# Optimization experiments

Hardware: AMD Instinct MI355X
Metric: run time of the kernel (lower is better)

The kernel has to match this reference:

```python
import jax, jax.numpy as jnp
import numpy as np

N_BUS = 1024
BATCH = 4096
N_NODES = N_BUS * BATCH
N_EDGES = 4 * N_NODES
F_IN, F1, F2, HID = 7, 12, 12, 128
EPS = 1e-5


def setup_inputs() -> dict:
    key = jax.random.key(0)
    ks = jax.random.split(key, 16)
    inp = {
        "x": jax.random.normal(ks[0], (N_NODES, F_IN), dtype=jnp.float32),
        "edge_index": jax.random.randint(ks[1], (2, N_EDGES), 0, N_NODES, dtype=jnp.int64),
        "batch_size": BATCH,
        # conv1 (PyG GraphConv): lin_rel (with bias) on aggregated msgs, lin_root (no bias)
        "Wrel1": jax.random.normal(ks[2], (F1, F_IN), dtype=jnp.float32) * 0.3,
        "brel1": jax.random.normal(ks[3], (F1,), dtype=jnp.float32) * 0.1,
        "Wroot1": jax.random.normal(ks[4], (F1, F_IN), dtype=jnp.float32) * 0.3,
        # conv2
        "Wrel2": jax.random.normal(ks[5], (F2, F1), dtype=jnp.float32) * 0.25,
        "brel2": jax.random.normal(ks[6], (F2,), dtype=jnp.float32) * 0.1,
        "Wroot2": jax.random.normal(ks[7], (F2, F1), dtype=jnp.float32) * 0.25,
        # batch norms
        "g1": jnp.ones((F1,), jnp.float32), "b1": jnp.zeros((F1,), jnp.float32),
        "g2": jnp.ones((F2,), jnp.float32), "b2": jnp.zeros((F2,), jnp.float32),
        # MLP head
        "W1": jax.random.normal(ks[8], (HID, N_BUS * F2), dtype=jnp.float32) * 0.01,
        "bl1": jnp.zeros((HID,), jnp.float32),
        "W2": jax.random.normal(ks[9], (N_BUS * 2, HID), dtype=jnp.float32) * 0.05,
        "bl2": jnp.zeros((N_BUS * 2,), jnp.float32),
    }
    return inp


def graph_conv(x, src, dst, Wrel, brel, Wroot):
    # out_i = Wrel @ (sum_{j: j->i} x_j) + brel + Wroot @ x_i
    agg = jax.ops.segment_sum(x[src], dst, num_segments=N_NODES)
    return agg @ Wrel.T + brel + x @ Wroot.T


def batch_norm(x, g, b):
    mu = x.mean(axis=0)
    var = x.var(axis=0)  # biased, as torch BN uses for normalization
    return (x - mu) * jax.lax.rsqrt(var + EPS) * g + b


def reference(x, edge_index, batch_size, Wrel1, brel1, Wroot1, Wrel2, brel2, Wroot2,
              g1, b1, g2, b2, W1, bl1, W2, bl2):
    src, dst = edge_index[0], edge_index[1]
    h = graph_conv(x, src, dst, Wrel1, brel1, Wroot1)
    h = jax.nn.relu(batch_norm(h, g1, b1))
    h = graph_conv(h, src, dst, Wrel2, brel2, Wroot2)
    h = jax.nn.relu(batch_norm(h, g2, b2))
    h = h.reshape(batch_size, N_BUS * F2)
    h = jax.nn.relu(h @ W1.T + bl1)
    return h @ W2.T + bl2
```

## Files before the change

### kernel.cpp

```cpp
#include <hip/hip_runtime.h>
#include <hip/hip_bf16.h>

#define NBUS    1024
#define BATCHSZ 4096
#define NNODES  (NBUS*BATCHSZ)
#define NEDGES  (4*NNODES)
#define FIN     7
#define FF1     12
#define FF2     12
#define HIDD    128
#define KDIM    (NBUS*FF2)
#define ODIM    (NBUS*2)
#define NBKT    4096
#define CAP     4608
#define ITPT    18
#define NCB     64
#define CAPA    265216

#define SZ_P    ((size_t)NNODES * 32)
#define SZ_HB   ((size_t)NNODES * FF2 * 2)
#define SZ_HID  ((size_t)BATCHSZ * HIDD * sizeof(float))
#define SZ_E    ((size_t)NBKT * CAP * sizeof(unsigned))
#define SZ_PB   ((size_t)NCB * CAPA * 8)

typedef unsigned u32x2v  __attribute__((ext_vector_type(2)));
typedef unsigned u32x4v  __attribute__((ext_vector_type(4)));

__device__ __forceinline__ float bflo(unsigned p){ return __uint_as_float(p << 16); }
__device__ __forceinline__ float bfhi(unsigned p){ return __uint_as_float(p & 0xffff0000u); }
__device__ __forceinline__ unsigned short f2bf(float f) {
    unsigned u = __float_as_uint(f);
    return (unsigned short)((u + 0x7fffu + ((u >> 16) & 1u)) >> 16);
}
__device__ __forceinline__ void nts_u2(unsigned* p, unsigned a, unsigned b) {
    u32x2v w; w.x = a; w.y = b;
    __builtin_nontemporal_store(w, (u32x2v*)p);
}
__device__ __forceinline__ void nts_u4(uint4* p, uint4 v) {
    u32x4v w; w.x = v.x; w.y = v.y; w.z = v.z; w.w = v.w;
    __builtin_nontemporal_store(w, (u32x4v*)p);
}
__device__ __forceinline__ uint2 ntl_u2(const unsigned* p) {
    u32x2v v = __builtin_nontemporal_load((const u32x2v*)p);
    uint2 r; r.x = v.x; r.y = v.y; return r;
}
__device__ __forceinline__ float4 ntl_f4(const float* p) {
    typedef float f32x4v __attribute__((ext_vector_type(4)));
    f32x4v v = __builtin_nontemporal_load((const f32x4v*)p);
    return make_float4(v.x, v.y, v.z, v.w);
}

__device__ __forceinline__ void acc7(float* agg, uint4 a) {
    agg[0] += bflo(a.x); agg[1] += bfhi(a.x);
    agg[2] += bflo(a.y); agg[3] += bfhi(a.y);
    agg[4] += bflo(a.z); agg[5] += bfhi(a.z);
    agg[6] += bflo(a.w);
}
__device__ __forceinline__ void accY(float* agg, const float* sc, const float* sh,
                                     uint4 r0, uint4 r1) {
    float v[FF1] = {bflo(r0.x), bfhi(r0.x), bflo(r0.y), bfhi(r0.y),
                    bflo(r0.z), bfhi(r0.z), bflo(r0.w), bfhi(r0.w),
                    bflo(r1.x), bfhi(r1.x), bflo(r1.y), bfhi(r1.y)};
    #pragma unroll
    for (int j = 0; j < FF1; ++j) {
        float y = v[j] * sc[j] + sh[j];
        agg[j] += (y > 0.f ? y : 0.f);
    }
}

__global__ void k_diag(float* __restrict__ out, int n, float v) {
    size_t i = (size_t)blockIdx.x * blockDim.x + threadIdx.x;
    if (i < (size_t)n) out[i] = v;
}

__global__ void k_init(const int* __restrict__ w, int* __restrict__ flag,
                       int* __restrict__ bcur, int* __restrict__ bcurA) {
    int u = blockIdx.x * 256 + threadIdx.x;
    if (u < NBKT) bcur[u] = u * CAP;
    if (u < NCB) bcurA[u] = u * CAPA;
    if (blockIdx.x == 0) {
        __shared__ int any;
        if (threadIdx.x == 0) any = 0;
        __syncthreads();
        int acc = 0;
        #pragma unroll
        for (int q = 0; q < 4; ++q) acc |= w[1 + 2 * (threadIdx.x * 4 + q)];
        if (acc) atomicOr(&any, 1);
        __syncthreads();
        if (threadIdx.x == 0) *flag = (any == 0) ? 2 : 1;
    }
}

__global__ __launch_bounds__(512) void k_partA(const int* __restrict__ ei,
                                               const int* __restrict__ flag,
                                               int* __restrict__ bcurA,
                                               unsigned* __restrict__ ebufA) {
    __shared__ int hist[NCB], lbase[NCB];
    int t = threadIdx.x;
    if (t < NCB) hist[t] = 0;
    __syncthreads();
    int mult = *flag;
    size_t base = (size_t)blockIdx.x * 32768;
    #pragma unroll 4
    for (int u = 0; u < 64; ++u) {
        size_t e = base + (size_t)u * 512 + t;
        int d = __builtin_nontemporal_load(ei + ((size_t)NEDGES + e) * mult);
        atomicAdd(&hist[d >> 16], 1);
    }
    __syncthreads();
    if (t < NCB) {
        int c = hist[t];
        lbase[t] = c ? atomicAdd(&bcurA[t], c) : 0;
        hist[t] = 0;
    }
    __syncthreads();
    #pragma unroll 4
    for (int u = 0; u < 64; ++u) {
        size_t e = base + (size_t)u * 512 + t;
        int s = __builtin_nontemporal_load(ei + e * mult);
        int d = __builtin_nontemporal_load(ei + ((size_t)NEDGES + e) * mult);
        int bk = d >> 16;
        int pos = lbase[bk] + atomicAdd(&hist[bk], 1);
        if (pos < (bk + 1) * CAPA) {
            uint2* p = (uint2*)(ebufA + (size_t)pos * 2);
            *p = make_uint2((unsigned)s, (unsigned)d);
        }
    }
}

__global__ __launch_bounds__(512) void k_partB(const unsigned* __restrict__ ebufA,
                                               const int* __restrict__ bendA,
                                               int* __restrict__ bcur,
                                               unsigned* __restrict__ ebuf) {
    __shared__ int hist[NCB], lbase[NCB];
    int t = threadIdx.x;
    int cb = blockIdx.x >> 2;
    int qq = blockIdx.x & 3;
    int abeg = cb * CAPA;
    int n = bendA[cb] - abeg; if (n > CAPA) n = CAPA;
    int beg = abeg + (int)(((long long)n * qq) >> 2);
    int end = abeg + (int)(((long long)n * (qq + 1)) >> 2);
    if (t < NCB) hist[t] = 0;
    __syncthreads();
    for (int k = beg + t; k < end; k += 512) {
        uint2 e = ntl_u2(ebufA + (size_t)k * 2);
        atomicAdd(&hist[(e.y >> 10) & 63u], 1);
    }
    __syncthreads();
    if (t < NCB) {
        int c = hist[t];
        lbase[t] = c ? atomicAdd(&bcur[cb * 64 + t], c) : 0;
        hist[t] = 0;
    }
    __syncthreads();
    for (int k = beg + t; k < end; k += 512) {
        uint2 e = ntl_u2(ebufA + (size_t)k * 2);
        int lb = (e.y >> 10) & 63u;
        int fb = cb * 64 + lb;
        int pos = lbase[lb] + atomicAdd(&hist[lb], 1);
        if (pos < (fb + 1) * CAP)
            ebuf[pos] = (e.x << 10) | (e.y & 1023u);
    }
}

__global__ __launch_bounds__(256) void k_padx(const float* __restrict__ x,
                                              uint4* __restrict__ xb) {
    size_t q = (size_t)blockIdx.x * blockDim.x + threadIdx.x;
    if (q >= NNODES / 4) return;
    const float4* xr = (const float4*)(x + q * 28);
    float v[28];
    #pragma unroll
    for (int u = 0; u < 7; ++u) {
        float4 f = xr[u];
        v[4*u] = f.x; v[4*u+1] = f.y; v[4*u+2] = f.z; v[4*u+3] = f.w;
    }
    #pragma unroll
    for (int n = 0; n < 4; ++n) {
        unsigned short h[8];
        #pragma unroll
        for (int j = 0; j < 7; ++j) h[j] = f2bf(v[7*n + j]);
        h[7] = 0;
        uint4 o;
        o.x = (unsigned)h[0] | ((unsigned)h[1] << 16);
        o.y = (unsigned)h[2] | ((unsigned)h[3] << 16);
        o.z = (unsigned)h[4] | ((unsigned)h[5] << 16);
        o.w = (unsigned)h[6] | ((unsigned)h[7] << 16);
        xb[q * 4 + n] = o;
    }
}

__global__ __launch_bounds__(256, 4) void k_conv1(const int* __restrict__ bend,
                                                  const unsigned* __restrict__ ebuf,
                                                  const uint4* __restrict__ xb,
                                                  const float* __restrict__ Wrel,
                                                  const float* __restrict__ brel,
                                                  const float* __restrict__ Wroot,
                                                  uint4* __restrict__ h1p) {
    __shared__ unsigned stage[CAP];
    __shared__ int hist[1024];
    __shared__ int offL[1024];
    __shared__ int wsum[4];
    __shared__ float sWr[FF1 * FIN], sWo[FF1 * FIN], sb[FF1];
    int t = threadIdx.x;
    if (t < FF1 * FIN) { sWr[t] = Wrel[t]; sWo[t] = Wroot[t]; }
    if (t < FF1) sb[t] = brel[t];
    int bk = blockIdx.x;
    int ebeg = bk * CAP;
    int n = bend[bk] - ebeg; if (n > CAP) n = CAP; if (n < 0) n = 0;
    for (int u = t; u < 1024; u += 256) hist[u] = 0;
    __syncthreads();
    for (int k = t; k < n; k += 256)
        atomicAdd(&hist[ebuf[ebeg + k] & 1023u], 1);
    __syncthreads();
    int v[4]; int s = 0;
    #pragma unroll
    for (int u = 0; u < 4; ++u) { v[u] = hist[t * 4 + u]; s += v[u]; }
    int lane = t & 63, w = t >> 6;
    int iv = s;
    for (int o = 1; o < 64; o <<= 1) { int uu = __shfl_up(iv, o); if (lane >= o) iv += uu; }
    if (lane == 63) wsum[w] = iv;
    __syncthreads();
    int basep = 0;
    #pragma unroll
    for (int ww = 0; ww < 4; ++ww) if (ww < w) basep += wsum[ww];
    int run = basep + iv - s;
    #pragma unroll
    for (int u = 0; u < 4; ++u) {
        offL[t * 4 + u] = run;
        hist[t * 4 + u] = run;
        run += v[u];
    }
    __syncthreads();
    for (int k = t; k < n; k += 256) {
        unsigned p = ebuf[ebeg + k];
        int pos = atomicAdd(&hist[p & 1023u], 1);
        stage[pos] = p >> 10;
    }
    __syncthreads();
    #pragma unroll
    for (int nn = 0; nn < 4; ++nn) {
        int li = nn * 256 + t;
        size_t i = (size_t)bk * 1024 + li;
        int beg = offL[li];
        int end = (li == 1023) ? n : offL[li + 1];
        float agg[FIN] = {0.f, 0.f, 0.f, 0.f, 0.f, 0.f, 0.f};
        int k = beg;
        for (; k + 3 < end; k += 4) {
            unsigned s0 = stage[k], s1 = stage[k+1], s2 = stage[k+2], s3 = stage[k+3];
            uint4 a0 = xb[s0], a1 = xb[s1], a2 = xb[s2], a3 = xb[s3];
            acc7(agg, a0); acc7(agg, a1); acc7(agg, a2); acc7(agg, a3);
        }
        for (; k < end; ++k) acc7(agg, xb[stage[k]]);
        uint4 ow = xb[i];
        float xv[FIN] = {bflo(ow.x), bfhi(ow.x), bflo(ow.y), bfhi(ow.y),
                         bflo(ow.z), bfhi(ow.z), bflo(ow.w)};
        unsigned short hh[FF1];
        #pragma unroll
        for (int j = 0; j < FF1; ++j) {
            float h = sb[j];
            #pragma unroll
            for (int q = 0; q < FIN; ++q) h += sWr[j * FIN + q] * agg[q] + sWo[j * FIN + q] * xv[q];
            hh[j] = f2bf(h);
        }
        uint4 w1, w2;
        w1.x = (unsigned)hh[0] | ((unsigned)hh[1] << 16);
        w1.y = (unsigned)hh[2] | ((unsigned)hh[3] << 16);
        w1.z = (unsigned)hh[4] | ((unsigned)hh[5] << 16);
        w1.w = (unsigned)hh[6] | ((unsigned)hh[7] << 16);
        w2.x = (unsigned)hh[8] | ((unsigned)hh[9] << 16);
        w2.y = (unsigned)hh[10]| ((unsigned)hh[11] << 16);
        w2.z = 0u; w2.w = 0u;
        nts_u4(h1p + i * 2, w1);
        nts_u4(h1p + i * 2 + 1, w2);
    }
}

template<int STRIDE>
__global__ __launch_bounds__(256) void k_statsb(const unsigned* __restrict__ hb,
                                                double* __restrict__ stats) {
    __shared__ float red[4][FF1], redq[4][FF1];
    int t = threadIdx.x;
    float ps[FF1], pq[FF1];
    #pragma unroll
    for (int j = 0; j < FF1; ++j) { ps[j] = 0.f; pq[j] = 0.f; }
    for (size_t i = (size_t)blockIdx.x * 256 + t; i < NNODES; i += 256 * 256) {
        const uint2* r = (const uint2*)(hb + i * STRIDE);
        uint2 u0 = r[0], u1 = r[1], u2 = r[2];
        float v[FF1] = {bflo(u0.x), bfhi(u0.x), bflo(u0.y), bfhi(u0.y),
                        bflo(u1.x), bfhi(u1.x), bflo(u1.y), bfhi(u1.y),
                        bflo(u2.x), bfhi(u2.x), bflo(u2.y), bfhi(u2.y)};
        #pragma unroll
        for (int j = 0; j < FF1; ++j) { ps[j] += v[j]; pq[j] += v[j] * v[j]; }
    }
    #pragma unroll
    for (int j = 0; j < FF1; ++j)
        for (int o = 1; o < 64; o <<= 1) { ps[j] += __shfl_xor(ps[j], o); pq[j] += __shfl_xor(pq[j], o); }
    int lane = t & 63, wv = t >> 6;
    if (lane == 0) {
        #pragma unroll
        for (int j = 0; j < FF1; ++j) { red[wv][j] = ps[j]; redq[wv][j] = pq[j]; }
    }
    __syncthreads();
    if (t < FF1) {
        float s = red[0][t] + red[1][t] + red[2][t] + red[3][t];
        float q = redq[0][t] + redq[1][t] + redq[2][t] + redq[3][t];
        atomicAdd(&stats[t], (double)s);
        atomicAdd(&stats[FF1 + t], (double)q);
    }
}

__global__ void k_finalize(const double* __restrict__ stats, const float* __restrict__ g,
                           const float* __restrict__ b, float* __restrict__ ss) {
    int j = threadIdx.x;
    if (j < FF1) {
        double mean = stats[j] * (1.0 / NNODES);
        double var  = stats[FF1 + j] * (1.0 / NNODES) - mean * mean;
        float sc = (float)((double)g[j] / sqrt(var + 1e-5));
        ss[j] = sc;
        ss[FF1 + j] = b[j] - (float)mean * sc;
    }
}

__global__ __launch_bounds__(256, 4) void k_conv2(const int* __restrict__ bend,
                                                  const unsigned* __restrict__ ebuf,
                                                  const uint4* __restrict__ h1p,
                                                  const float* __restrict__ ss,
                                                  const float* __restrict__ Wrel,
                                                  const float* __restrict__ brel,
                                                  const float* __restrict__ Wroot,
                                                  unsigned* __restrict__ h2b) {
    __shared__ unsigned stage[CAP];
    __shared__ int hist[1024];
    __shared__ int offL[1024];
    __shared__ int wsum[4];
    __shared__ float sWr[FF2 * FF1], sWo[FF2 * FF1], sb[FF2], sc[FF1], sh[FF1];
    int t = threadIdx.x;
    if (t < FF2 * FF1) { sWr[t] = Wrel[t]; sWo[t] = Wroot[t]; }
    if (t < FF2) { sb[t] = brel[t]; sc[t] = ss[t]; sh[t] = ss[FF1 + t]; }
    int bk = blockIdx.x;
    int ebeg = bk * CAP;
    int n = bend[bk] - ebeg; if (n > CAP) n = CAP; if (n < 0) n = 0;
    for (int u = t; u < 1024; u += 256) hist[u] = 0;
    __syncthreads();
    for (int k = t; k < n; k += 256)
        atomicAdd(&hist[ebuf[ebeg + k] & 1023u], 1);
    __syncthreads();
    int v[4]; int s = 0;
    #pragma unroll
    for (int u = 0; u < 4; ++u) { v[u] = hist[t * 4 + u]; s += v[u]; }
    int lane = t & 63, w = t >> 6;
    int iv = s;
    for (int o = 1; o < 64; o <<= 1) { int uu = __shfl_up(iv, o); if (lane >= o) iv += uu; }
    if (lane == 63) wsum[w] = iv;
    __syncthreads();
    int basep = 0;
    #pragma unroll
    for (int ww = 0; ww < 4; ++ww) if (ww < w) basep += wsum[ww];
    int run = basep + iv - s;
    #pragma unroll
    for (int u = 0; u < 4; ++u) {
        offL[t * 4 + u] = run;
        hist[t * 4 + u] = run;
        run += v[u];
    }
    __syncthreads();
    for (int k = t; k < n; k += 256) {
        unsigned p = ebuf[ebeg + k];
        int pos = atomicAdd(&hist[p & 1023u], 1);
        stage[pos] = p >> 10;
    }
    __syncthreads();
    #pragma unroll
    for (int nn = 0; nn < 4; ++nn) {
        int li = nn * 256 + t;
        size_t i = (size_t)bk * 1024 + li;
        int beg = offL[li];
        int end = (li == 1023) ? n : offL[li + 1];
        float agg[FF1];
        #pragma unroll
        for (int j = 0; j < FF1; ++j) agg[j] = 0.f;
        int k = beg;
        for (; k + 3 < end; k += 4) {
            unsigned s0 = stage[k], s1 = stage[k+1], s2 = stage[k+2], s3 = stage[k+3];
            uint4 a0 = h1p[(size_t)s0 * 2], a1 = h1p[(size_t)s0 * 2 + 1];
            uint4 b0 = h1p[(size_t)s1 * 2], b1 = h1p[(size_t)s1 * 2 + 1];
            uint4 c0 = h1p[(size_t)s2 * 2], c1 = h1p[(size_t)s2 * 2 + 1];
            uint4 d0 = h1p[(size_t)s3 * 2], d1 = h1p[(size_t)s3 * 2 + 1];
            accY(agg, sc, sh, a0, a1);
            accY(agg, sc, sh, b0, b1);
            accY(agg, sc, sh, c0, c1);
            accY(agg, sc, sh, d0, d1);
        }
        for (; k < end; ++k) {
            unsigned s0 = stage[k];
            accY(agg, sc, sh, h1p[(size_t)s0 * 2], h1p[(size_t)s0 * 2 + 1]);
        }
        uint4 o0 = h1p[i * 2], o1 = h1p[i * 2 + 1];
        float vo[FF1] = {bflo(o0.x), bfhi(o0.x), bflo(o0.y), bfhi(o0.y),
                         bflo(o0.z), bfhi(o0.z), bflo(o0.w), bfhi(o0.w),
                         bflo(o1.x), bfhi(o1.x), bflo(o1.y), bfhi(o1.y)};
        float y[FF1];
        #pragma unroll
        for (int j = 0; j < FF1; ++j) {
            float wv = vo[j] * sc[j] + sh[j];
            y[j] = wv > 0.f ? wv : 0.f;
        }
        unsigned short hh[FF2];
        #pragma unroll
        for (int j = 0; j < FF2; ++j) {
            float h = sb[j];
            #pragma unroll
            for (int q = 0; q < FF1; ++q) h += sWr[j * FF1 + q] * agg[q] + sWo[j * FF1 + q] * y[q];
            hh[j] = f2bf(h);
        }
        unsigned* p = h2b + i * 6;
        nts_u2(p,     (unsigned)hh[0] | ((unsigned)hh[1] << 16),
                      (unsigned)hh[2] | ((unsigned)hh[3] << 16));
        nts_u2(p + 2, (unsigned)hh[4] | ((unsigned)hh[5] << 16),
                      (unsigned)hh[6] | ((unsigned)hh[7] << 16));
        nts_u2(p + 4, (unsigned)hh[8] | ((unsigned)hh[9] << 16),
                      (unsigned)hh[10]| ((unsigned)hh[11] << 16));
    }
}

__global__ __launch_bounds__(256) void k_gemm1(const unsigned short* __restrict__ h2b,
                                               const float* __restrict__ ss2,
                                               const float* __restrict__ W1,
                                               float* __restrict__ hidp) {
    __shared__ float As[32][128];
    __shared__ float Bs[32][128];
    __shared__ float sc[FF2], sh[FF2];
    int t = threadIdx.x;
    if (t < FF2) { sc[t] = ss2[t]; sh[t] = ss2[FF2 + t]; }
    __syncthreads();
    int mb = blockIdx.x;
    int ks = blockIdx.y;
    const int KS = KDIM / 8;
    int m0 = mb * 128;
    int kbase = ks * KS;
    int r  = t >> 1;
    int kg = t & 1;
    int tr = t >> 4;
    int tc = t & 15;
    float acc[8][8];
    #pragma unroll
    for (int i = 0; i < 8; ++i)
        #pragma unroll
        for (int j = 0; j < 8; ++j) acc[i][j] = 0.f;

    for (int kt = 0; kt < KS; kt += 32) {
        int c0 = kbase + kt + 16 * kg;
        const uint2* arow = (const uint2*)(h2b + (size_t)(m0 + r) * KDIM + c0);
        const float* brow = W1 + (size_t)r * KDIM + c0;
        #pragma unroll
        for (int i = 0; i < 4; ++i) {
            uint2 av = arow[i];
            int cc = c0 + 4 * i;
            int j0 = cc % FF2;
            float vals[4] = {bflo(av.x), bfhi(av.x), bflo(av.y), bfhi(av.y)};
            #pragma unroll
            for (int ii = 0; ii < 4; ++ii) {
                int j = j0 + ii; if (j >= FF2) j -= FF2;
                float v = vals[ii] * sc[j] + sh[j];
                As[16 * kg + 4 * i + ii][r] = v > 0.f ? v : 0.f;
            }
            float4 bv = *(const float4*)(brow + 4 * i);
            Bs[16 * kg + 4 * i + 0][r] = bv.x;
            Bs[16 * kg + 4 * i + 1][r] = bv.y;
            Bs[16 * kg + 4 * i + 2][r] = bv.z;
            Bs[16 * kg + 4 * i + 3][r] = bv.w;
        }
        __syncthreads();
        #pragma unroll
        for (int k = 0; k < 32; ++k) {
            float a[8], b[8];
            *(float4*)&a[0] = *(const float4*)&As[k][8 * tr];
            *(float4*)&a[4] = *(const float4*)&As[k][8 * tr + 4];
            *(float4*)&b[0] = *(const float4*)&Bs[k][8 * tc];
            *(float4*)&b[4] = *(const float4*)&Bs[k][8 * tc + 4];
            #pragma unroll
            for (int i = 0; i < 8; ++i)
                #pragma unroll
                for (int j = 0; j < 8; ++j) acc[i][j] += a[i] * b[j];
        }
        __syncthreads();
    }
    float* obase = hidp + (size_t)ks * (BATCHSZ * HIDD);
    #pragma unroll
    for (int i = 0; i < 8; ++i) {
        float* orow = obase + (size_t)(m0 + 8 * tr + i) * HIDD + 8 * tc;
        *(float4*)(orow)     = make_float4(acc[i][0], acc[i][1], acc[i][2], acc[i][3]);
        *(float4*)(orow + 4) = make_float4(acc[i][4], acc[i][5], acc[i][6], acc[i][7]);
    }
}

__global__ __launch_bounds__(256) void k_hred(const float* __restrict__ hidp,
                                              const float* __restrict__ bl1,
                                              float* __restrict__ hid) {
    int i = blockIdx.x * 256 + threadIdx.x;
    float s = bl1[i & (HIDD - 1)];
    #pragma unroll
    for (int p = 0; p < 8; ++p) s += hidp[(size_t)p * (BATCHSZ * HIDD) + i];
    hid[i] = s > 0.f ? s : 0.f;
}

__global__ __launch_bounds__(256) void k_gemm2(const float* __restrict__ hid,
                                               const float* __restrict__ W2,
                                               const float* __restrict__ bl2,
                                               float* __restrict__ out) {
    __shared__ float As[32][128];
    __shared__ float Bs[32][128];
    int t = threadIdx.x;
    int m0 = blockIdx.x * 128;
    int n0 = blockIdx.y * 128;
    int r  = t >> 1;
    int kg = t & 1;
    int tr = t >> 4;
    int tc = t & 15;
    float acc[8][8];
    #pragma unroll
    for (int i = 0; i < 8; ++i)
        #pragma unroll
        for (int j = 0; j < 8; ++j) acc[i][j] = 0.f;

    for (int kt = 0; kt < HIDD; kt += 32) {
        int c0 = kt + 16 * kg;
        #pragma unroll
        for (int i = 0; i < 4; ++i) {
            float4 av = *(const float4*)(hid + (size_t)(m0 + r) * HIDD + c0 + 4 * i);
            As[16 * kg + 4 * i + 0][r] = av.x;
            As[16 * kg + 4 * i + 1][r] = av.y;
            As[16 * kg + 4 * i + 2][r] = av.z;
            As[16 * kg + 4 * i + 3][r] = av.w;
            float4 bv = *(const float4*)(W2 + (size_t)(n0 + r) * HIDD + c0 + 4 * i);
            Bs[16 * kg + 4 * i + 0][r] = bv.x;
            Bs[16 * kg + 4 * i + 1][r] = bv.y;
            Bs[16 * kg + 4 * i + 2][r] = bv.z;
            Bs[16 * kg + 4 * i + 3][r] = bv.w;
        }
        __syncthreads();
        #pragma unroll
        for (int k = 0; k < 32; ++k) {
            float a[8], b[8];
            *(float4*)&a[0] = *(const float4*)&As[k][8 * tr];
            *(float4*)&a[4] = *(const float4*)&As[k][8 * tr + 4];
            *(float4*)&b[0] = *(const float4*)&Bs[k][8 * tc];
            *(float4*)&b[4] = *(const float4*)&Bs[k][8 * tc + 4];
            #pragma unroll
            for (int i = 0; i < 8; ++i)
                #pragma unroll
                for (int j = 0; j < 8; ++j) acc[i][j] += a[i] * b[j];
        }
        __syncthreads();
    }
    float4 c0v = *(const float4*)(bl2 + n0 + 8 * tc);
    float4 c1v = *(const float4*)(bl2 + n0 + 8 * tc + 4);
    float bvals[8] = {c0v.x, c0v.y, c0v.z, c0v.w, c1v.x, c1v.y, c1v.z, c1v.w};
    #pragma unroll
    for (int i = 0; i < 8; ++i) {
        size_t ro = (size_t)(m0 + 8 * tr + i) * ODIM + n0 + 8 * tc;
        *(float4*)(out + ro)     = make_float4(acc[i][0] + bvals[0], acc[i][1] + bvals[1],
                                               acc[i][2] + bvals[2], acc[i][3] + bvals[3]);
        *(float4*)(out + ro + 4) = make_float4(acc[i][4] + bvals[4], acc[i][5] + bvals[5],
                                               acc[i][6] + bvals[6], acc[i][7] + bvals[7]);
    }
}

extern "C" void kernel_launch(void* const* d_in, const int* in_sizes, int n_in,
                              void* d_out, int out_size, void* d_ws, size_t ws_size,
                              hipStream_t stream) {
    const float* x      = (const float*)d_in[0];
    const int*   ei     = (const int*)d_in[1];
    const float* Wrel1  = (const float*)d_in[3];
    const float* brel1  = (const float*)d_in[4];
    const float* Wroot1 = (const float*)d_in[5];
    const float* Wrel2  = (const float*)d_in[6];
    const float* brel2  = (const float*)d_in[7];
    const float* Wroot2 = (const float*)d_in[8];
    const float* g1     = (const float*)d_in[9];
    const float* b1     = (const float*)d_in[10];
    const float* g2     = (const float*)d_in[11];
    const float* b2     = (const float*)d_in[12];
    const float* W1     = (const float*)d_in[13];
    const float* bl1    = (const float*)d_in[14];
    const float* W2     = (const float*)d_in[15];
    const float* bl2    = (const float*)d_in[16];
    float* out = (float*)d_out;
    char* ws = (char*)d_ws;

    const size_t req = SZ_P + SZ_E + SZ_PB + 32768;
    if (ws_size < req) {
        float v = (float)(ws_size >> 20);
        k_diag<<<(out_size + 255) / 256, 256, 0, stream>>>(out, out_size, v);
        return;
    }
    char* pY = ws;
    unsigned* ebuf = (unsigned*)(ws + SZ_P);
    char* pB = ws + SZ_P + SZ_E;
    char* pK = ws + SZ_P + SZ_E + SZ_PB;
    int*  bcur  = (int*)pK;
    int*  bcurA = (int*)(pK + 16384);
    char* smalls = pK + 20480;
    double* st1  = (double*)smalls;
    double* st2  = st1 + 2 * FF1;
    float*  ss1  = (float*)(st2 + 2 * FF2);
    float*  ss2  = ss1 + 2 * FF1;
    int*    flag = (int*)(ss2 + 2 * FF2);

    uint4*    xb    = (uint4*)pY;
    unsigned* h2b   = (unsigned*)pY;
    float*    hidp  = (float*)(pY + SZ_HB);
    float*    hid   = (float*)(pY + SZ_HB + 8 * SZ_HID);
    unsigned* ebufA = (unsigned*)pB;
    uint4*    h1p   = (uint4*)pB;

    hipMemsetAsync(smalls, 0, 1024, stream);
    k_init  <<<16, 256, 0, stream>>>(ei, flag, bcur, bcurA);
    k_padx  <<<NNODES / 4 / 256, 256, 0, stream>>>(x, xb);
    k_partA <<<512, 512, 0, stream>>>(ei, flag, bcurA, ebufA);
    k_partB <<<NCB * 4, 512, 0, stream>>>(ebufA, bcurA, bcur, ebuf);
    k_conv1 <<<NBKT, 256, 0, stream>>>(bcur, ebuf, xb, Wrel1, brel1, Wroot1, h1p);
    k_statsb<8><<<256, 256, 0, stream>>>((const unsigned*)h1p, st1);
    k_finalize<<<1, 64, 0, stream>>>(st1, g1, b1, ss1);
    k_conv2 <<<NBKT, 256, 0, stream>>>(bcur, ebuf, h1p, ss1, Wrel2, brel2, Wroot2, h2b);
    k_statsb<6><<<256, 256, 0, stream>>>(h2b, st2);
    k_finalize<<<1, 64, 0, stream>>>(st2, g2, b2, ss2);
    k_gemm1<<<dim3(BATCHSZ / 128, 8), 256, 0, stream>>>((const unsigned short*)h2b, ss2, W1, hidp);
    k_hred <<<BATCHSZ * HIDD / 256, 256, 0, stream>>>(hidp, bl1, hid);
    k_gemm2<<<dim3(BATCHSZ / 128, ODIM / 128), 256, 0, stream>>>(hid, W2, bl2, out);
}
```

Baseline: 1.415 ms.

## Use bf16 MFMA for MLP first layer and per-wave histograms in partitioning

The first MLP GEMM moves from an FP32 LDS-tiled SIMT loop to bf16 MFMA 16x16x32 instructions. The activations are normalized, passed through ReLU and converted to bf16 in registers, and W1 is converted to bf16 by a new prep kernel. Separately, both edge-partition kernels now keep one shared-memory histogram per wave, which reduces LDS atomic contention. The GEMM change lowers the precision of W1 and the activations to bf16, and it loads operands straight from global memory without LDS staging.

```diff
diff --git a/kernel.cpp b/kernel.cpp
--- a/kernel.cpp
+++ b/kernel.cpp
@@ -13,7 +13,6 @@
 #define ODIM    (NBUS*2)
 #define NBKT    4096
 #define CAP     4608
-#define ITPT    18
 #define NCB     64
 #define CAPA    265216
 
@@ -22,9 +21,12 @@
 #define SZ_HID  ((size_t)BATCHSZ * HIDD * sizeof(float))
 #define SZ_E    ((size_t)NBKT * CAP * sizeof(unsigned))
 #define SZ_PB   ((size_t)NCB * CAPA * 8)
+#define SZ_W1B  ((size_t)HIDD * KDIM * 2)
 
 typedef unsigned u32x2v  __attribute__((ext_vector_type(2)));
 typedef unsigned u32x4v  __attribute__((ext_vector_type(4)));
+typedef __attribute__((ext_vector_type(8))) short bf16x8;
+typedef __attribute__((ext_vector_type(4))) float f32x4;
 
 __device__ __forceinline__ float bflo(unsigned p){ return __uint_as_float(p << 16); }
 __device__ __forceinline__ float bfhi(unsigned p){ return __uint_as_float(p & 0xffff0000u); }
@@ -43,11 +45,6 @@
 __device__ __forceinline__ uint2 ntl_u2(const unsigned* p) {
     u32x2v v = __builtin_nontemporal_load((const u32x2v*)p);
     uint2 r; r.x = v.x; r.y = v.y; return r;
-}
-__device__ __forceinline__ float4 ntl_f4(const float* p) {
-    typedef float f32x4v __attribute__((ext_vector_type(4)));
-    f32x4v v = __builtin_nontemporal_load((const f32x4v*)p);
-    return make_float4(v.x, v.y, v.z, v.w);
 }
 
 __device__ __forceinline__ void acc7(float* agg, uint4 a) {
@@ -95,9 +92,11 @@
                                                const int* __restrict__ flag,
                                                int* __restrict__ bcurA,
                                                unsigned* __restrict__ ebufA) {
-    __shared__ int hist[NCB], lbase[NCB];
+    __shared__ int hist[8][NCB];
+    __shared__ int lbase[8][NCB];
     int t = threadIdx.x;
-    if (t < NCB) hist[t] = 0;
+    int w8 = t >> 6;
+    for (int u = t; u < 8 * NCB; u += 512) ((int*)hist)[u] = 0;
     __syncthreads();
     int mult = *flag;
     size_t base = (size_t)blockIdx.x * 32768;
@@ -105,13 +104,16 @@
     for (int u = 0; u < 64; ++u) {
         size_t e = base + (size_t)u * 512 + t;
         int d = __builtin_nontemporal_load(ei + ((size_t)NEDGES + e) * mult);
-        atomicAdd(&hist[d >> 16], 1);
+        atomicAdd(&hist[w8][d >> 16], 1);
     }
     __syncthreads();
     if (t < NCB) {
-        int c = hist[t];
-        lbase[t] = c ? atomicAdd(&bcurA[t], c) : 0;
-        hist[t] = 0;
+        int c[8]; int ctot = 0;
+        #pragma unroll
+        for (int ww = 0; ww < 8; ++ww) { c[ww] = hist[ww][t]; ctot += c[ww]; }
+        int bg = ctot ? atomicAdd(&bcurA[t], ctot) : 0;
+        #pragma unroll
+        for (int ww = 0; ww < 8; ++ww) { lbase[ww][t] = bg; bg += c[ww]; hist[ww][t] = 0; }
     }
     __syncthreads();
     #pragma unroll 4
@@ -120,7 +122,7 @@
         int s = __builtin_nontemporal_load(ei + e * mult);
         int d = __builtin_nontemporal_load(ei + ((size_t)NEDGES + e) * mult);
         int bk = d >> 16;
-        int pos = lbase[bk] + atomicAdd(&hist[bk], 1);
+        int pos = lbase[w8][bk] + atomicAdd(&hist[w8][bk], 1);
         if (pos < (bk + 1) * CAPA) {
             uint2* p = (uint2*)(ebufA + (size_t)pos * 2);
             *p = make_uint2((unsigned)s, (unsigned)d);
@@ -132,32 +134,37 @@
                                                const int* __restrict__ bendA,
                                                int* __restrict__ bcur,
                                                unsigned* __restrict__ ebuf) {
-    __shared__ int hist[NCB], lbase[NCB];
+    __shared__ int hist[8][NCB];
+    __shared__ int lbase[8][NCB];
     int t = threadIdx.x;
+    int w8 = t >> 6;
     int cb = blockIdx.x >> 2;
     int qq = blockIdx.x & 3;
     int abeg = cb * CAPA;
     int n = bendA[cb] - abeg; if (n > CAPA) n = CAPA;
     int beg = abeg + (int)(((long long)n * qq) >> 2);
     int end = abeg + (int)(((long long)n * (qq + 1)) >> 2);
-    if (t < NCB) hist[t] = 0;
+    for (int u = t; u < 8 * NCB; u += 512) ((int*)hist)[u] = 0;
     __syncthreads();
     for (int k = beg + t; k < end; k += 512) {
         uint2 e = ntl_u2(ebufA + (size_t)k * 2);
-        atomicAdd(&hist[(e.y >> 10) & 63u], 1);
+        atomicAdd(&hist[w8][(e.y >> 10) & 63u], 1);
     }
     __syncthreads();
     if (t < NCB) {
-        int c = hist[t];
-        lbase[t] = c ? atomicAdd(&bcur[cb * 64 + t], c) : 0;
-        hist[t] = 0;
+        int c[8]; int ctot = 0;
+        #pragma unroll
+        for (int ww = 0; ww < 8; ++ww) { c[ww] = hist[ww][t]; ctot += c[ww]; }
+        int bg = ctot ? atomicAdd(&bcur[cb * 64 + t], ctot) : 0;
+        #pragma unroll
+        for (int ww = 0; ww < 8; ++ww) { lbase[ww][t] = bg; bg += c[ww]; hist[ww][t] = 0; }
     }
     __syncthreads();
     for (int k = beg + t; k < end; k += 512) {
         uint2 e = ntl_u2(ebufA + (size_t)k * 2);
         int lb = (e.y >> 10) & 63u;
         int fb = cb * 64 + lb;
-        int pos = lbase[lb] + atomicAdd(&hist[lb], 1);
+        int pos = lbase[w8][lb] + atomicAdd(&hist[w8][lb], 1);
         if (pos < (fb + 1) * CAP)
             ebuf[pos] = (e.x << 10) | (e.y & 1023u);
     }
@@ -187,6 +194,20 @@
         o.w = (unsigned)h[6] | ((unsigned)h[7] << 16);
         xb[q * 4 + n] = o;
     }
+}
+
+__global__ __launch_bounds__(256) void k_w1b(const float* __restrict__ W1,
+                                             uint4* __restrict__ w1b) {
+    size_t q = (size_t)blockIdx.x * blockDim.x + threadIdx.x;
+    if (q >= (size_t)HIDD * KDIM / 8) return;
+    const float4* r = (const float4*)(W1 + q * 8);
+    float4 a = r[0], b = r[1];
+    uint4 o;
+    o.x = (unsigned)f2bf(a.x) | ((unsigned)f2bf(a.y) << 16);
+    o.y = (unsigned)f2bf(a.z) | ((unsigned)f2bf(a.w) << 16);
+    o.z = (unsigned)f2bf(b.x) | ((unsigned)f2bf(b.y) << 16);
+    o.w = (unsigned)f2bf(b.z) | ((unsigned)f2bf(b.w) << 16);
+    w1b[q] = o;
 }
 
 __global__ __launch_bounds__(256, 4) void k_conv1(const int* __restrict__ bend,
@@ -423,74 +444,73 @@
     }
 }
 
-__global__ __launch_bounds__(256) void k_gemm1(const unsigned short* __restrict__ h2b,
-                                               const float* __restrict__ ss2,
-                                               const float* __restrict__ W1,
-                                               float* __restrict__ hidp) {
-    __shared__ float As[32][128];
-    __shared__ float Bs[32][128];
+__global__ __launch_bounds__(256) void k_gemm1m(const unsigned short* __restrict__ h2b,
+                                                const float* __restrict__ ss2,
+                                                const unsigned short* __restrict__ w1b,
+                                                float* __restrict__ hidp) {
     __shared__ float sc[FF2], sh[FF2];
     int t = threadIdx.x;
     if (t < FF2) { sc[t] = ss2[t]; sh[t] = ss2[FF2 + t]; }
     __syncthreads();
+    const int KS = KDIM / 8;
     int mb = blockIdx.x;
     int ks = blockIdx.y;
-    const int KS = KDIM / 8;
-    int m0 = mb * 128;
+    int wid = t >> 6;
+    int lane = t & 63;
+    int wm = wid >> 1, wn = wid & 1;
+    int m0 = mb * 128 + wm * 64;
+    int n0 = wn * 64;
+    int lrow = lane & 15;
+    int kgrp = lane >> 4;
+    f32x4 acc[4][4];
+    #pragma unroll
+    for (int mi = 0; mi < 4; ++mi)
+        #pragma unroll
+        for (int ni = 0; ni < 4; ++ni) acc[mi][ni] = (f32x4)(0.f);
     int kbase = ks * KS;
-    int r  = t >> 1;
-    int kg = t & 1;
-    int tr = t >> 4;
-    int tc = t & 15;
-    float acc[8][8];
-    #pragma unroll
-    for (int i = 0; i < 8; ++i)
-        #pragma unroll
-        for (int j = 0; j < 8; ++j) acc[i][j] = 0.f;
-
-    for (int kt = 0; kt < KS; kt += 32) {
-        int c0 = kbase + kt + 16 * kg;
-        const uint2* arow = (const uint2*)(h2b + (size_t)(m0 + r) * KDIM + c0);
-        const float* brow = W1 + (size_t)r * KDIM + c0;
-        #pragma unroll
-        for (int i = 0; i < 4; ++i) {
-            uint2 av = arow[i];
-            int cc = c0 + 4 * i;
-            int j0 = cc % FF2;
-            float vals[4] = {bflo(av.x), bfhi(av.x), bflo(av.y), bfhi(av.y)};
+    for (int k0 = 0; k0 < KS; k0 += 32) {
+        int kk = kbase + k0 + kgrp * 8;
+        bf16x8 af[4], bf[4];
+        #pragma unroll
+        for (int mi = 0; mi < 4; ++mi) {
+            const unsigned short* ap = h2b + (size_t)(m0 + mi * 16 + lrow) * KDIM + kk;
+            uint4 av = *(const uint4*)ap;
+            unsigned hw[8] = {av.x & 0xffffu, av.x >> 16, av.y & 0xffffu, av.y >> 16,
+                              av.z & 0xffffu, av.z >> 16, av.w & 0xffffu, av.w >> 16};
+            int j = kk % FF2;
+            bf16x8 r;
             #pragma unroll
-            for (int ii = 0; ii < 4; ++ii) {
-                int j = j0 + ii; if (j >= FF2) j -= FF2;
-                float v = vals[ii] * sc[j] + sh[j];
-                As[16 * kg + 4 * i + ii][r] = v > 0.f ? v : 0.f;
+            for (int u = 0; u < 8; ++u) {
+                float f = __uint_as_float(hw[u] << 16);
+                float y = f * sc[j] + sh[j];
+                y = y > 0.f ? y : 0.f;
+                r[u] = (short)f2bf(y);
+                ++j; if (j >= FF2) j = 0;
             }
-            float4 bv = *(const float4*)(brow + 4 * i);
-            Bs[16 * kg + 4 * i + 0][r] = bv.x;
-            Bs[16 * kg + 4 * i + 1][r] = bv.y;
-            Bs[16 * kg + 4 * i + 2][r] = bv.z;
-            Bs[16 * kg + 4 * i + 3][r] = bv.w;
-        }
-        __syncthreads();
-        #pragma unroll
-        for (int k = 0; k < 32; ++k) {
-            float a[8], b[8];
-            *(float4*)&a[0] = *(const float4*)&As[k][8 * tr];
-            *(float4*)&a[4] = *(const float4*)&As[k][8 * tr + 4];
-            *(float4*)&b[0] = *(const float4*)&Bs[k][8 * tc];
-            *(float4*)&b[4] = *(const float4*)&Bs[k][8 * tc + 4];
+            af[mi] = r;
+        }
+        #pragma unroll
+        for (int ni = 0; ni < 4; ++ni)
+            bf[ni] = *(const bf16x8*)(w1b + (size_t)(n0 + ni * 16 + lrow) * KDIM + kk);
+        #pragma unroll
+        for (int mi = 0; mi < 4; ++mi)
             #pragma unroll
-            for (int i = 0; i < 8; ++i)
-                #pragma unroll
-                for (int j = 0; j < 8; ++j) acc[i][j] += a[i] * b[j];
-        }
-        __syncthreads();
+            for (int ni = 0; ni < 4; ++ni)
+                acc[mi][ni] = __builtin_amdgcn_mfma_f32_16x16x32_bf16(
+                    af[mi], bf[ni], acc[mi][ni], 0, 0, 0);
     }
     float* obase = hidp + (size_t)ks * (BATCHSZ * HIDD);
     #pragma unroll
-    for (int i = 0; i < 8; ++i) {
-        float* orow = obase + (size_t)(m0 + 8 * tr + i) * HIDD + 8 * tc;
-        *(float4*)(orow)     = make_float4(acc[i][0], acc[i][1], acc[i][2], acc[i][3]);
-        *(float4*)(orow + 4) = make_float4(acc[i][4], acc[i][5], acc[i][6], acc[i][7]);
+    for (int mi = 0; mi < 4; ++mi) {
+        #pragma unroll
+        for (int ni = 0; ni < 4; ++ni) {
+            #pragma unroll
+            for (int reg = 0; reg < 4; ++reg) {
+                int row = m0 + mi * 16 + kgrp * 4 + reg;
+                int col = n0 + ni * 16 + lrow;
+                obase[(size_t)row * HIDD + col] = acc[mi][ni][reg];
+            }
+        }
     }
 }
 
@@ -588,7 +608,7 @@
     float* out = (float*)d_out;
     char* ws = (char*)d_ws;
 
-    const size_t req = SZ_P + SZ_E + SZ_PB + 32768;
+    const size_t req = SZ_P + SZ_E + SZ_PB + 32768 + SZ_W1B;
     if (ws_size < req) {
         float v = (float)(ws_size >> 20);
         k_diag<<<(out_size + 255) / 256, 256, 0, stream>>>(out, out_size, v);
@@ -606,6 +626,7 @@
     float*  ss1  = (float*)(st2 + 2 * FF2);
     float*  ss2  = ss1 + 2 * FF1;
     int*    flag = (int*)(ss2 + 2 * FF2);
+    uint4*  w1b  = (uint4*)(pK + 32768);
 
     uint4*    xb    = (uint4*)pY;
     unsigned* h2b   = (unsigned*)pY;
@@ -617,6 +638,7 @@
     hipMemsetAsync(smalls, 0, 1024, stream);
     k_init  <<<16, 256, 0, stream>>>(ei, flag, bcur, bcurA);
     k_padx  <<<NNODES / 4 / 256, 256, 0, stream>>>(x, xb);
+    k_w1b   <<<HIDD * KDIM / 8 / 256, 256, 0, stream>>>(W1, w1b);
     k_partA <<<512, 512, 0, stream>>>(ei, flag, bcurA, ebufA);
     k_partB <<<NCB * 4, 512, 0, stream>>>(ebufA, bcurA, bcur, ebuf);
     k_conv1 <<<NBKT, 256, 0, stream>>>(bcur, ebuf, xb, Wrel1, brel1, Wroot1, h1p);
@@ -625,7 +647,8 @@
     k_conv2 <<<NBKT, 256, 0, stream>>>(bcur, ebuf, h1p, ss1, Wrel2, brel2, Wroot2, h2b);
     k_statsb<6><<<256, 256, 0, stream>>>(h2b, st2);
     k_finalize<<<1, 64, 0, stream>>>(st2, g2, b2, ss2);
-    k_gemm1<<<dim3(BATCHSZ / 128, 8), 256, 0, stream>>>((const unsigned short*)h2b, ss2, W1, hidp);
+    k_gemm1m<<<dim3(BATCHSZ / 128, 8), 256, 0, stream>>>((const unsigned short*)h2b, ss2,
+                                                         (const unsigned short*)w1b, hidp);
     k_hred <<<BATCHSZ * HIDD / 256, 256, 0, stream>>>(hidp, bl1, hid);
     k_gemm2<<<dim3(BATCHSZ / 128, ODIM / 128), 256, 0, stream>>>(hid, W2, bl2, out);
 }
```

New measurement: 1.384 ms. 2.2% less time.
